# Kernel tuning notes

Measured on AMD Instinct MI355X. Metric: run time of the kernel, lower is better.

## Reference

```python
import jax, jax.numpy as jnp
import numpy as np

N_NODES = 100000
N_EDGES = 1200000
EDGE_OUT = 64
HID = 256
NODE_OUT = 128
N_GRAPHS = 16


def setup_inputs() -> dict:
    key = jax.random.key(0)
    ks = jax.random.split(key, 8)
    x = jax.random.normal(ks[0], (N_NODES, 7), dtype=jnp.float32)
    edge_index = jax.random.randint(ks[1], (2, N_EDGES), 0, N_NODES, dtype=jnp.int64)
    edge_attr = jax.random.normal(ks[2], (N_EDGES, EDGE_OUT), dtype=jnp.float32)
    u = jax.random.normal(ks[3], (N_GRAPHS, 1), dtype=jnp.float32)
    batch = jax.random.randint(ks[4], (N_NODES,), 0, N_GRAPHS, dtype=jnp.int64)
    fan_in = 3 * EDGE_OUT + 1  # 193
    W1 = jax.random.normal(ks[5], (fan_in, HID), dtype=jnp.float32) / np.sqrt(fan_in)
    b1 = jnp.zeros((HID,), dtype=jnp.float32)
    W2 = jax.random.normal(ks[6], (HID, NODE_OUT), dtype=jnp.float32) / np.sqrt(HID)
    b2 = jnp.zeros((NODE_OUT,), dtype=jnp.float32)
    return {"x": x, "edge_index": edge_index, "edge_attr": edge_attr, "u": u,
            "batch": batch, "W1": W1, "b1": b1, "W2": W2, "b2": b2}


def reference(x, edge_index, edge_attr, u, batch, W1, b1, W2, b2):
    N = x.shape[0]
    col = edge_index[1]
    # scatter_add
    out1 = jax.ops.segment_sum(edge_attr, col, num_segments=N)  # [N, edge_out]
    # scatter_max; empty segments -> 0 (torch_scatter semantics)
    out2 = jax.ops.segment_max(edge_attr, col, num_segments=N)
    cnt = jax.ops.segment_sum(jnp.ones((edge_attr.shape[0],), edge_attr.dtype), col,
                              num_segments=N)[:, None]  # [N, 1]
    out2 = jnp.where(cnt > 0, out2, 0.0)
    # scatter_mean
    out3 = out1 / jnp.maximum(cnt, 1.0)
    feat = jnp.concatenate([out1, out2, out3, u[batch]], axis=1)  # [N, 3*edge_out+1]
    h = jax.nn.gelu(feat @ W1 + b1, approximate=False)  # exact GELU, as torch default
    return h @ W2 + b2  # [N, node_out]
```

## Files before the change

### kernel.cpp

```cpp
#include <hip/hip_runtime.h>
#include <hip/hip_bf16.h>
#include <math.h>

#define N_NODES 100000
#define N_EDGES 1200000
#define EO      64
#define HID     256
#define NOUT    128
#define KP      224
#define TILE_R  64
#define HSTR    264
#define PCAP    1280

typedef __attribute__((ext_vector_type(8))) short bf16x8;
typedef __attribute__((ext_vector_type(4))) float f32x4;

__device__ __forceinline__ short f2bf(float x) {
    __hip_bfloat16 h = __float2bfloat16(x);
    return *reinterpret_cast<short*>(&h);
}

__device__ __forceinline__ f32x4 max4(f32x4 a, f32x4 b) {
    f32x4 r;
    r.x = fmaxf(a.x, b.x); r.y = fmaxf(a.y, b.y);
    r.z = fmaxf(a.z, b.z); r.w = fmaxf(a.w, b.w);
    return r;
}

__global__ void prep_k(const float* __restrict__ W1, const float* __restrict__ W2,
                       short* __restrict__ W1T, short* __restrict__ W2T) {
    int i = blockIdx.x * 256 + threadIdx.x;
    if (i < HID * KP) {
        int n = i / KP, k = i - n * KP;
        W1T[i] = (k < 193) ? f2bf(W1[k * HID + n]) : (short)0;
    } else {
        int j = i - HID * KP;
        if (j < NOUT * HID) {
            int n = j / HID, k = j - n * HID;
            W2T[j] = f2bf(W2[k * NOUT + n]);
        }
    }
}

__global__ void hist_k(const int* __restrict__ ei, unsigned* __restrict__ hist) {
    int e = blockIdx.x * 256 + threadIdx.x;
    if (e < N_EDGES) atomicAdd(&hist[ei[N_EDGES + e]], 1u);
}

__global__ void scan_part_k(unsigned* __restrict__ off, unsigned* __restrict__ bsum) {
    __shared__ unsigned s[256];
    int t = threadIdx.x, i = blockIdx.x * 256 + t;
    unsigned v = (i < N_NODES) ? off[i] : 0u;
    s[t] = v; __syncthreads();
    for (int d = 1; d < 256; d <<= 1) {
        unsigned x = (t >= d) ? s[t - d] : 0u; __syncthreads();
        s[t] += x; __syncthreads();
    }
    if (i < N_NODES) off[i] = s[t] - v;
    if (t == 255) bsum[blockIdx.x] = s[255];
}

__global__ void scan_top_k(const unsigned* __restrict__ bsum, unsigned* __restrict__ boff, int nb) {
    __shared__ unsigned s[512];
    int t = threadIdx.x;
    unsigned v = (t < nb) ? bsum[t] : 0u;
    s[t] = v; __syncthreads();
    for (int d = 1; d < 512; d <<= 1) {
        unsigned x = (t >= d) ? s[t - d] : 0u; __syncthreads();
        s[t] += x; __syncthreads();
    }
    boff[t] = s[t] - v;
}

__global__ void scan_add_k(unsigned* __restrict__ off, const unsigned* __restrict__ boff,
                           unsigned* __restrict__ cursor) {
    int i = blockIdx.x * 256 + threadIdx.x;
    if (i < N_NODES) {
        unsigned o = off[i] + boff[blockIdx.x];
        off[i] = o; cursor[i] = o;
    }
}

__global__ void place_k(const int* __restrict__ ei, unsigned* __restrict__ cursor,
                        unsigned* __restrict__ perm) {
    int e = blockIdx.x * 256 + threadIdx.x;
    if (e < N_EDGES) {
        int c = ei[N_EDGES + e];
        unsigned p = atomicAdd(&cursor[c], 1u);
        perm[p] = (unsigned)e;
    }
}

__launch_bounds__(256)
__global__ void fused_k(const unsigned* __restrict__ off, const unsigned* __restrict__ perm,
                        const float* __restrict__ ea, const float* __restrict__ u,
                        const int* __restrict__ batch,
                        const short* __restrict__ W1T, const short* __restrict__ W2T,
                        const float* __restrict__ b1, const float* __restrict__ b2,
                        float* __restrict__ out) {
    __shared__ short smem[TILE_R * HSTR];
    __shared__ unsigned offs[TILE_R + 1];
    __shared__ float uvals[TILE_R];
    __shared__ unsigned perms[PCAP];

    const int tid = threadIdx.x;
    const int w = tid >> 6;
    const int lane = tid & 63;
    const int row_base = blockIdx.x * TILE_R;

    if (tid <= TILE_R) {
        const int n = row_base + tid;
        offs[tid] = (n < N_NODES) ? off[n] : (unsigned)N_EDGES;
    }
    if (tid < TILE_R) {
        const int n = row_base + tid;
        uvals[tid] = (n < N_NODES) ? u[batch[n]] : 0.0f;
    }
    __syncthreads();
    const unsigned s0 = offs[0];
    const int T = (int)(offs[TILE_R] - s0);
    const int Tst = T < PCAP ? T : PCAP;
    for (int j = tid; j < Tst; j += 256) perms[j] = perm[s0 + j];
    __syncthreads();

    const int g  = lane >> 4;
    const int fo = (lane & 15) * 4;
    const f32x4 z4 = {0.0f, 0.0f, 0.0f, 0.0f};
    const f32x4 ninf4 = {-INFINITY, -INFINITY, -INFINITY, -INFINITY};

#define ACC_LOOP(LD)                                                        \
    {                                                                       \
        int p = es + g;                                                     \
        for (; p + 4 < ee; p += 8) {                                        \
            const int e0 = (int)LD(p);                                      \
            const int e1 = (int)LD(p + 4);                                  \
            const f32x4 v0 = *(const f32x4*)&ea[(size_t)e0 * EO + fo];      \
            const f32x4 v1 = *(const f32x4*)&ea[(size_t)e1 * EO + fo];      \
            sa += v0; ma = max4(ma, v0);                                    \
            sb += v1; mb = max4(mb, v1);                                    \
        }                                                                   \
        if (p < ee) {                                                       \
            const int e0 = (int)LD(p);                                      \
            const f32x4 v0 = *(const f32x4*)&ea[(size_t)e0 * EO + fo];      \
            sa += v0; ma = max4(ma, v0);                                    \
        }                                                                   \
    }
#define LDS_LD(pp) (perms[(pp)])
#define GLB_LD(pp) (perm[s0 + (pp)])

    for (int i = 0; i < 16; ++i) {
        const int rl = w * 16 + i;
        const int n = row_base + rl;
        short* frow = &smem[rl * KP];
        if (n < N_NODES) {
            const int es  = (int)(offs[rl] - s0);
            const int ee  = (int)(offs[rl + 1] - s0);
            const int deg = ee - es;

            f32x4 sa = z4, sb = z4;
            f32x4 ma = ninf4, mb = ninf4;
            if (ee <= PCAP) {
                ACC_LOOP(LDS_LD)
            } else {
                ACC_LOOP(GLB_LD)
            }
            sa += sb; ma = max4(ma, mb);

            #pragma unroll
            for (int j = 0; j < 4; ++j) {
                float s = sa[j], m = ma[j];
                s += __shfl_xor(s, 16); m = fmaxf(m, __shfl_xor(m, 16));
                s += __shfl_xor(s, 32); m = fmaxf(m, __shfl_xor(m, 32));
                sa[j] = s; ma[j] = m;
            }

            const float rdeg = 1.0f / fmaxf((float)deg, 1.0f);
            if (g == 0) {
                #pragma unroll
                for (int j = 0; j < 4; ++j) frow[fo + j] = f2bf(sa[j]);
            } else if (g == 1) {
                #pragma unroll
                for (int j = 0; j < 4; ++j)
                    frow[EO + fo + j] = f2bf(deg > 0 ? ma[j] : 0.0f);
            } else if (g == 2) {
                #pragma unroll
                for (int j = 0; j < 4; ++j) frow[2 * EO + fo + j] = f2bf(sa[j] * rdeg);
            } else {
                const int c = (lane & 15) * 2;
                frow[192 + c]     = (c == 0) ? f2bf(uvals[rl]) : (short)0;
                frow[192 + c + 1] = (short)0;
            }
        } else {
            frow[lane] = 0; frow[EO + lane] = 0; frow[2 * EO + lane] = 0;
            if (lane < 32) frow[192 + lane] = 0;
        }
    }
    __syncthreads();

    const int m = lane & 15, q = lane >> 4;
    const f32x4 vzero = {0.0f, 0.0f, 0.0f, 0.0f};

    f32x4 acc1[4][4];
    #pragma unroll
    for (int a = 0; a < 4; ++a)
        #pragma unroll
        for (int b = 0; b < 4; ++b) acc1[a][b] = vzero;

    for (int kk = 0; kk < 7; ++kk) {
        const int k0 = kk * 32;
        bf16x8 afr[4];
        #pragma unroll
        for (int mt = 0; mt < 4; ++mt)
            afr[mt] = *(const bf16x8*)&smem[(mt * 16 + m) * KP + k0 + q * 8];
        #pragma unroll
        for (int ct = 0; ct < 4; ++ct) {
            const int col = w * 64 + ct * 16 + m;
            bf16x8 bfr = *(const bf16x8*)&W1T[col * KP + k0 + q * 8];
            #pragma unroll
            for (int mt = 0; mt < 4; ++mt)
                acc1[mt][ct] = __builtin_amdgcn_mfma_f32_16x16x32_bf16(afr[mt], bfr, acc1[mt][ct], 0, 0, 0);
        }
    }
    __syncthreads();

    #pragma unroll
    for (int ct = 0; ct < 4; ++ct) {
        const int col = w * 64 + ct * 16 + m;
        const float bv = b1[col];
        #pragma unroll
        for (int mt = 0; mt < 4; ++mt) {
            #pragma unroll
            for (int i = 0; i < 4; ++i) {
                float t = acc1[mt][ct][i] + bv;
                t = 0.5f * t * (1.0f + erff(t * 0.70710678118654752f));
                smem[(mt * 16 + q * 4 + i) * HSTR + col] = f2bf(t);
            }
        }
    }
    __syncthreads();

    f32x4 acc2[4][2];
    #pragma unroll
    for (int a = 0; a < 4; ++a) { acc2[a][0] = vzero; acc2[a][1] = vzero; }

    for (int kk = 0; kk < 8; ++kk) {
        const int k0 = kk * 32;
        bf16x8 afr[4];
        #pragma unroll
        for (int mt = 0; mt < 4; ++mt)
            afr[mt] = *(const bf16x8*)&smem[(mt * 16 + m) * HSTR + k0 + q * 8];
        #pragma unroll
        for (int ct = 0; ct < 2; ++ct) {
            const int col = w * 32 + ct * 16 + m;
            bf16x8 bfr = *(const bf16x8*)&W2T[col * HID + k0 + q * 8];
            #pragma unroll
            for (int mt = 0; mt < 4; ++mt)
                acc2[mt][ct] = __builtin_amdgcn_mfma_f32_16x16x32_bf16(afr[mt], bfr, acc2[mt][ct], 0, 0, 0);
        }
    }

    #pragma unroll
    for (int ct = 0; ct < 2; ++ct) {
        const int col = w * 32 + ct * 16 + m;
        const float bv = b2[col];
        #pragma unroll
        for (int mt = 0; mt < 4; ++mt) {
            #pragma unroll
            for (int i = 0; i < 4; ++i) {
                const int row = row_base + mt * 16 + q * 4 + i;
                if (row < N_NODES) out[(size_t)row * NOUT + col] = acc2[mt][ct][i] + bv;
            }
        }
    }
}

extern "C" void kernel_launch(void* const* d_in, const int* in_sizes, int n_in,
                              void* d_out, int out_size, void* d_ws, size_t ws_size,
                              hipStream_t stream) {
    const int*   ei    = (const int*)d_in[1];
    const float* ea    = (const float*)d_in[2];
    const float* u     = (const float*)d_in[3];
    const int*   batch = (const int*)d_in[4];
    const float* W1    = (const float*)d_in[5];
    const float* b1    = (const float*)d_in[6];
    const float* W2    = (const float*)d_in[7];
    const float* b2    = (const float*)d_in[8];
    float* out = (float*)d_out;

    unsigned* off    = (unsigned*)d_ws;
    unsigned* cursor = off + N_NODES;
    unsigned* perm   = cursor + N_NODES;
    unsigned* bsum   = perm + N_EDGES;
    unsigned* boff   = bsum + 512;
    short*    W1T    = (short*)(boff + 512);
    short*    W2T    = W1T + HID * KP;

    const int NB = (N_NODES + 255) / 256;

    hipMemsetAsync(off, 0, (size_t)N_NODES * 4, stream);
    prep_k<<<(HID * KP + NOUT * HID + 255) / 256, 256, 0, stream>>>(W1, W2, W1T, W2T);
    hist_k<<<(N_EDGES + 255) / 256, 256, 0, stream>>>(ei, off);
    scan_part_k<<<NB, 256, 0, stream>>>(off, bsum);
    scan_top_k<<<1, 512, 0, stream>>>(bsum, boff, NB);
    scan_add_k<<<NB, 256, 0, stream>>>(off, boff, cursor);
    place_k<<<(N_EDGES + 255) / 256, 256, 0, stream>>>(ei, cursor, perm);
    fused_k<<<(N_NODES + TILE_R - 1) / TILE_R, 256, 0, stream>>>(
        off, perm, ea, u, batch, W1T, W2T, b1, b2, out);
}
```

Baseline: 697.8 us.

## Map one node per 16-lane group in gather, vectorize histogram/placement edge reads

The fused kernel's aggregation phase now gives each 16-lane group its own node, so a wave processes four nodes at once. Before, the whole wave split one node's edges four ways and combined the partials with cross-lane shuffles. Each group walks its node's edge list with four independent accumulators, which removes the shuffle reductions and the per-group branching on what to write. The trade-off is load imbalance when nodes in the same wave have different degrees. The histogram and placement kernels now read four destination indices per thread through one int4 load and launch a quarter as many threads.

```diff
diff --git a/kernel.cpp b/kernel.cpp
--- a/kernel.cpp
+++ b/kernel.cpp
@@ -43,8 +43,14 @@
 }
 
 __global__ void hist_k(const int* __restrict__ ei, unsigned* __restrict__ hist) {
-    int e = blockIdx.x * 256 + threadIdx.x;
-    if (e < N_EDGES) atomicAdd(&hist[ei[N_EDGES + e]], 1u);
+    int e4 = (blockIdx.x * 256 + threadIdx.x) * 4;
+    if (e4 < N_EDGES) {
+        const int4 c = *(const int4*)&ei[N_EDGES + e4];
+        atomicAdd(&hist[c.x], 1u);
+        atomicAdd(&hist[c.y], 1u);
+        atomicAdd(&hist[c.z], 1u);
+        atomicAdd(&hist[c.w], 1u);
+    }
 }
 
 __global__ void scan_part_k(unsigned* __restrict__ off, unsigned* __restrict__ bsum) {
@@ -83,11 +89,13 @@
 
 __global__ void place_k(const int* __restrict__ ei, unsigned* __restrict__ cursor,
                         unsigned* __restrict__ perm) {
-    int e = blockIdx.x * 256 + threadIdx.x;
-    if (e < N_EDGES) {
-        int c = ei[N_EDGES + e];
-        unsigned p = atomicAdd(&cursor[c], 1u);
-        perm[p] = (unsigned)e;
+    int e4 = (blockIdx.x * 256 + threadIdx.x) * 4;
+    if (e4 < N_EDGES) {
+        const int4 c = *(const int4*)&ei[N_EDGES + e4];
+        unsigned p0 = atomicAdd(&cursor[c.x], 1u); perm[p0] = (unsigned)(e4);
+        unsigned p1 = atomicAdd(&cursor[c.y], 1u); perm[p1] = (unsigned)(e4 + 1);
+        unsigned p2 = atomicAdd(&cursor[c.z], 1u); perm[p2] = (unsigned)(e4 + 2);
+        unsigned p3 = atomicAdd(&cursor[c.w], 1u); perm[p3] = (unsigned)(e4 + 3);
     }
 }
 
@@ -123,77 +131,70 @@
     for (int j = tid; j < Tst; j += 256) perms[j] = perm[s0 + j];
     __syncthreads();
 
-    const int g  = lane >> 4;
-    const int fo = (lane & 15) * 4;
+    const int g16 = lane >> 4;
+    const int fo  = (lane & 15) * 4;
     const f32x4 z4 = {0.0f, 0.0f, 0.0f, 0.0f};
     const f32x4 ninf4 = {-INFINITY, -INFINITY, -INFINITY, -INFINITY};
 
-#define ACC_LOOP(LD)                                                        \
+#define GATHER_LOOP(LD)                                                     \
     {                                                                       \
-        int p = es + g;                                                     \
-        for (; p + 4 < ee; p += 8) {                                        \
+        int p = es;                                                         \
+        for (; p + 3 < ee; p += 4) {                                        \
             const int e0 = (int)LD(p);                                      \
-            const int e1 = (int)LD(p + 4);                                  \
+            const int e1 = (int)LD(p + 1);                                  \
+            const int e2 = (int)LD(p + 2);                                  \
+            const int e3 = (int)LD(p + 3);                                  \
             const f32x4 v0 = *(const f32x4*)&ea[(size_t)e0 * EO + fo];      \
             const f32x4 v1 = *(const f32x4*)&ea[(size_t)e1 * EO + fo];      \
-            sa += v0; ma = max4(ma, v0);                                    \
-            sb += v1; mb = max4(mb, v1);                                    \
+            const f32x4 v2 = *(const f32x4*)&ea[(size_t)e2 * EO + fo];      \
+            const f32x4 v3 = *(const f32x4*)&ea[(size_t)e3 * EO + fo];      \
+            sv0 += v0; mv0 = max4(mv0, v0);                                 \
+            sv1 += v1; mv1 = max4(mv1, v1);                                 \
+            sv2 += v2; mv2 = max4(mv2, v2);                                 \
+            sv3 += v3; mv3 = max4(mv3, v3);                                 \
         }                                                                   \
-        if (p < ee) {                                                       \
+        for (; p < ee; ++p) {                                               \
             const int e0 = (int)LD(p);                                      \
             const f32x4 v0 = *(const f32x4*)&ea[(size_t)e0 * EO + fo];      \
-            sa += v0; ma = max4(ma, v0);                                    \
+            sv0 += v0; mv0 = max4(mv0, v0);                                 \
         }                                                                   \
     }
 #define LDS_LD(pp) (perms[(pp)])
 #define GLB_LD(pp) (perm[s0 + (pp)])
 
-    for (int i = 0; i < 16; ++i) {
-        const int rl = w * 16 + i;
-        const int n = row_base + rl;
+    for (int i = 0; i < 4; ++i) {
+        const int rl = w * 16 + i * 4 + g16;
+        const int es = (int)(offs[rl] - s0);
+        const int ee = (int)(offs[rl + 1] - s0);
+        const int deg = ee - es;
+
+        f32x4 sv0 = z4, sv1 = z4, sv2 = z4, sv3 = z4;
+        f32x4 mv0 = ninf4, mv1 = ninf4, mv2 = ninf4, mv3 = ninf4;
+        if (ee <= PCAP) {
+            GATHER_LOOP(LDS_LD)
+        } else {
+            GATHER_LOOP(GLB_LD)
+        }
+        const f32x4 sv = (sv0 + sv1) + (sv2 + sv3);
+        const f32x4 mv = max4(max4(mv0, mv1), max4(mv2, mv3));
+        const float rdeg = 1.0f / fmaxf((float)deg, 1.0f);
+
         short* frow = &smem[rl * KP];
-        if (n < N_NODES) {
-            const int es  = (int)(offs[rl] - s0);
-            const int ee  = (int)(offs[rl + 1] - s0);
-            const int deg = ee - es;
-
-            f32x4 sa = z4, sb = z4;
-            f32x4 ma = ninf4, mb = ninf4;
-            if (ee <= PCAP) {
-                ACC_LOOP(LDS_LD)
-            } else {
-                ACC_LOOP(GLB_LD)
-            }
-            sa += sb; ma = max4(ma, mb);
-
-            #pragma unroll
-            for (int j = 0; j < 4; ++j) {
-                float s = sa[j], m = ma[j];
-                s += __shfl_xor(s, 16); m = fmaxf(m, __shfl_xor(m, 16));
-                s += __shfl_xor(s, 32); m = fmaxf(m, __shfl_xor(m, 32));
-                sa[j] = s; ma[j] = m;
-            }
-
-            const float rdeg = 1.0f / fmaxf((float)deg, 1.0f);
-            if (g == 0) {
-                #pragma unroll
-                for (int j = 0; j < 4; ++j) frow[fo + j] = f2bf(sa[j]);
-            } else if (g == 1) {
-                #pragma unroll
-                for (int j = 0; j < 4; ++j)
-                    frow[EO + fo + j] = f2bf(deg > 0 ? ma[j] : 0.0f);
-            } else if (g == 2) {
-                #pragma unroll
-                for (int j = 0; j < 4; ++j) frow[2 * EO + fo + j] = f2bf(sa[j] * rdeg);
-            } else {
-                const int c = (lane & 15) * 2;
-                frow[192 + c]     = (c == 0) ? f2bf(uvals[rl]) : (short)0;
-                frow[192 + c + 1] = (short)0;
-            }
-        } else {
-            frow[lane] = 0; frow[EO + lane] = 0; frow[2 * EO + lane] = 0;
-            if (lane < 32) frow[192 + lane] = 0;
-        }
+        #pragma unroll
+        for (int j = 0; j < 4; ++j) {
+            frow[fo + j]          = f2bf(sv[j]);
+            frow[EO + fo + j]     = f2bf(deg > 0 ? mv[j] : 0.0f);
+            frow[2 * EO + fo + j] = f2bf(sv[j] * rdeg);
+        }
+    }
+
+    {
+        const int rl = w * 16 + (lane & 15);
+        short* frow = &smem[rl * KP];
+        const int c0 = 192 + g16 * 8;
+        #pragma unroll
+        for (int j = 0; j < 8; ++j)
+            frow[c0 + j] = (c0 + j == 192) ? f2bf(uvals[rl]) : (short)0;
     }
     __syncthreads();
 
@@ -299,11 +300,11 @@
 
     hipMemsetAsync(off, 0, (size_t)N_NODES * 4, stream);
     prep_k<<<(HID * KP + NOUT * HID + 255) / 256, 256, 0, stream>>>(W1, W2, W1T, W2T);
-    hist_k<<<(N_EDGES + 255) / 256, 256, 0, stream>>>(ei, off);
+    hist_k<<<(N_EDGES / 4 + 255) / 256, 256, 0, stream>>>(ei, off);
     scan_part_k<<<NB, 256, 0, stream>>>(off, bsum);
     scan_top_k<<<1, 512, 0, stream>>>(bsum, boff, NB);
     scan_add_k<<<NB, 256, 0, stream>>>(off, boff, cursor);
-    place_k<<<(N_EDGES + 255) / 256, 256, 0, stream>>>(ei, cursor, perm);
+    place_k<<<(N_EDGES / 4 + 255) / 256, 256, 0, stream>>>(ei, cursor, perm);
     fused_k<<<(N_NODES + TILE_R - 1) / TILE_R, 256, 0, stream>>>(
         off, perm, ea, u, batch, W1T, W2T, b1, b2, out);
 }
```

Measured after the change: 672.0 us. 1.04x faster.
